# Optimization experiments

Measured on AMD Instinct MI355X. Metric: run time of the kernel, lower is better.

Reference implementation:

```python
import jax, jax.numpy as jnp
import numpy as np

N_NODES = 50000


def gcn_layer(x, src, dst, W, b):
    # GCNConv: out = D^{-1/2} (A + I) D^{-1/2} (x W) + b
    n = x.shape[0]
    h = x @ W  # [N, C_out]
    # degree including self-loop (count of incoming edges at dst + 1)
    deg = jnp.zeros((n,), dtype=x.dtype).at[dst].add(1.0) + 1.0
    dinv_sqrt = jax.lax.rsqrt(deg)
    norm = dinv_sqrt[src] * dinv_sqrt[dst]  # [E]
    agg = jax.ops.segment_sum(h[src] * norm[:, None], dst, num_segments=n)
    # self-loop contribution: norm_ii = 1/deg_i
    agg = agg + h * (dinv_sqrt * dinv_sqrt)[:, None]
    return agg + b


def setup_inputs() -> dict:
    key = jax.random.key(0)
    k1, k2, k3, k4, k5, k6 = jax.random.split(key, 6)
    in_c, hid_c, out_c = 128, 128, 64
    x = jax.random.normal(k1, (N_NODES, in_c), dtype=jnp.float32)
    edge_index = jax.random.randint(k2, (2, 600000), 0, N_NODES, dtype=jnp.int64)
    W1 = jax.random.normal(k3, (in_c, hid_c), dtype=jnp.float32) * (1.0 / np.sqrt(in_c))
    b1 = jnp.zeros((hid_c,), dtype=jnp.float32)
    W2 = jax.random.normal(k4, (hid_c, out_c), dtype=jnp.float32) * (1.0 / np.sqrt(hid_c))
    b2 = jnp.zeros((out_c,), dtype=jnp.float32)
    return {"x": x, "edge_index": edge_index, "W1": W1, "b1": b1, "W2": W2, "b2": b2}


def reference(x, edge_index, W1, b1, W2, b2):
    src, dst = edge_index[0], edge_index[1]
    h = gcn_layer(x, src, dst, W1, b1)
    h = jax.nn.relu(h)
    out = gcn_layer(h, src, dst, W2, b2)
    return out
```

## Files before the change

### kernel.cpp

```cpp
#include <hip/hip_runtime.h>

#define IN_C 128
#define HID_C 128
#define OUT_C 64
#define CAP 40
#define LSTR 40

typedef unsigned int uint;
typedef unsigned short ushort;
typedef __attribute__((ext_vector_type(8))) short short8;
typedef __attribute__((ext_vector_type(4))) float f32x4;

__device__ __forceinline__ float bf2f(ushort u) {
    return __uint_as_float(((uint)u) << 16);
}
__device__ __forceinline__ float bfl(uint u) {
    return __uint_as_float(u << 16);
}
__device__ __forceinline__ float bfh(uint u) {
    return __uint_as_float(u & 0xffff0000u);
}
__device__ __forceinline__ ushort f2bf(float f) {
    uint u = __float_as_uint(f);
    return (ushort)((u + 0x7fffu + ((u >> 16) & 1u)) >> 16);
}


__global__ void prep0_kernel(int* __restrict__ cursor, int n,
                             const float* __restrict__ W1, ushort* __restrict__ w1h,
                             ushort* __restrict__ w1l, const float* __restrict__ W2,
                             ushort* __restrict__ w2h, ushort* __restrict__ w2l) {
    int idx = blockIdx.x * blockDim.x + threadIdx.x;
    if (idx < n) {
        cursor[idx] = 0;
    } else if (idx < n + 128 * 128) {
        int i1 = idx - n;
        int k = i1 >> 7, c = i1 & 127;
        float w = W1[i1];
        ushort h = f2bf(w);
        ushort l = f2bf(w - bf2f(h));
        w1h[c * 128 + k] = h;
        w1l[c * 128 + k] = l;
    } else if (idx < n + 128 * 128 + 128 * 64) {
        int i2 = idx - n - 128 * 128;
        int k = i2 >> 6, c = i2 & 63;
        float w = W2[i2];
        ushort h = f2bf(w);
        ushort l = f2bf(w - bf2f(h));
        w2h[c * 128 + k] = h;
        w2l[c * 128 + k] = l;
    }
}


__global__ __launch_bounds__(256) void gemm1_edge_kernel(
    const float* __restrict__ A, const ushort* __restrict__ BTh,
    const ushort* __restrict__ BTl, ushort* __restrict__ C, int M, int gblocks,
    const int* __restrict__ src, const int* __restrict__ dst,
    int* __restrict__ cursor, int* __restrict__ csr_src, int E) {
    constexpr int BN = 128;
    constexpr int NT = BN / 16;
    __shared__ ushort sAh[64 * LSTR], sAl[64 * LSTR];
    __shared__ ushort sBh[BN * LSTR], sBl[BN * LSTR];

    const int tid = threadIdx.x;

    if (blockIdx.x >= gblocks) {
        int e = (blockIdx.x - gblocks) * 256 + tid;
        if (e < E) {
            unsigned s = (unsigned)src[e];
            unsigned d = (unsigned)dst[e];
            if (s < (unsigned)M && d < (unsigned)M) {
                int p = atomicAdd(&cursor[d], 1);
                if (p < CAP) csr_src[d * CAP + p] = (int)s;
            }
        }
        return;
    }

    const int w = tid >> 6;
    const int lane = tid & 63;
    const int m = lane & 15;
    const int quad = lane >> 4;
    const int r0 = blockIdx.x * 64;

    f32x4 acc[NT];
#pragma unroll
    for (int t = 0; t < NT; ++t) acc[t] = (f32x4){0.f, 0.f, 0.f, 0.f};

    for (int k0 = 0; k0 < 128; k0 += 32) {
#pragma unroll
        for (int it = 0; it < 2; ++it) {
            int idx = tid + it * 256;
            int row = idx >> 3;
            int c4 = idx & 7;
            int grow = r0 + row;
            float4 v = make_float4(0.f, 0.f, 0.f, 0.f);
            if (grow < M) v = *(const float4*)&A[(size_t)grow * 128 + k0 + c4 * 4];
            ushort h0 = f2bf(v.x), h1 = f2bf(v.y), h2 = f2bf(v.z), h3 = f2bf(v.w);
            ushort l0 = f2bf(v.x - bf2f(h0)), l1 = f2bf(v.y - bf2f(h1));
            ushort l2 = f2bf(v.z - bf2f(h2)), l3 = f2bf(v.w - bf2f(h3));
            *(ushort4*)&sAh[row * LSTR + c4 * 4] = make_ushort4(h0, h1, h2, h3);
            *(ushort4*)&sAl[row * LSTR + c4 * 4] = make_ushort4(l0, l1, l2, l3);
        }
        for (int idx = tid; idx < BN * 4; idx += 256) {
            int row = idx >> 2;
            int c = idx & 3;
            *(uint4*)&sBh[row * LSTR + c * 8] = *(const uint4*)&BTh[row * 128 + k0 + c * 8];
            *(uint4*)&sBl[row * LSTR + c * 8] = *(const uint4*)&BTl[row * 128 + k0 + c * 8];
        }
        __syncthreads();

        short8 ah = *(const short8*)&sAh[(w * 16 + m) * LSTR + quad * 8];
        short8 al = *(const short8*)&sAl[(w * 16 + m) * LSTR + quad * 8];
#pragma unroll
        for (int t = 0; t < NT; ++t) {
            short8 bh = *(const short8*)&sBh[(t * 16 + m) * LSTR + quad * 8];
            short8 bl = *(const short8*)&sBl[(t * 16 + m) * LSTR + quad * 8];
            acc[t] = __builtin_amdgcn_mfma_f32_16x16x32_bf16(ah, bh, acc[t], 0, 0, 0);
            acc[t] = __builtin_amdgcn_mfma_f32_16x16x32_bf16(al, bh, acc[t], 0, 0, 0);
            acc[t] = __builtin_amdgcn_mfma_f32_16x16x32_bf16(ah, bl, acc[t], 0, 0, 0);
        }
        __syncthreads();
    }

#pragma unroll
    for (int t = 0; t < NT; ++t) {
#pragma unroll
        for (int r = 0; r < 4; ++r) {
            int row = r0 + w * 16 + quad * 4 + r;
            if (row < M) C[(size_t)row * BN + t * 16 + m] = f2bf(acc[t][r]);
        }
    }
}


#define ACC8(v, nn)                                     \
    {                                                   \
        a0 += (nn) * bfl((v).x); a1 += (nn) * bfh((v).x); \
        a2 += (nn) * bfl((v).y); a3 += (nn) * bfh((v).y); \
        a4 += (nn) * bfl((v).z); a5 += (nn) * bfh((v).z); \
        a6 += (nn) * bfl((v).w); a7 += (nn) * bfh((v).w); \
    }


__global__ __launch_bounds__(256) void agg_gemm2_kernel(
    const uint4* __restrict__ hx, const int* __restrict__ csr_src,
    const int* __restrict__ degs, const float* __restrict__ bias,
    const ushort* __restrict__ BTh, const ushort* __restrict__ BTl,
    ushort* __restrict__ C, int n) {
    __shared__ ushort sAf[4][32][LSTR];

    const int tid = threadIdx.x;
    const int w = tid >> 6;
    const int lane = tid & 63;
    const int q4 = lane >> 4;
    const int c16 = lane & 15;
    const int r0 = blockIdx.x * 32;

    int nd = 0, t0 = 0, t1 = 0, t2 = 0;
    {
        int node = r0 + w * 8 + q4;
        bool valid = node < n;
        nd = valid ? degs[node] : 0;
        size_t base = (size_t)node * CAP;
        t0 = valid ? csr_src[base + c16] : 0;
        t1 = valid ? csr_src[base + 16 + c16] : 0;
        t2 = (valid && c16 < 8) ? csr_src[base + 32 + c16] : 0;
    }

    for (int g = 0; g < 2; ++g) {
        const int lrow = w * 8 + g * 4 + q4;
        const int node = r0 + lrow;
        const bool valid = node < n;
        const int cnt = min(nd, CAP);
        const float degf = (float)(cnt + 1);
        const float dinv = rsqrtf(degf);
        int es0 = (c16 < cnt) ? t0 : 0;
        int es1 = (16 + c16 < cnt) ? t1 : 0;
        int es2 = (32 + c16 < cnt) ? t2 : 0;
        int d0 = degs[es0];
        int d1 = degs[es1];
        int d2 = degs[es2];
        uint4 sv = make_uint4(0u, 0u, 0u, 0u);
        if (valid) sv = hx[(size_t)node * 16 + c16];
        int nd_n = 0, t0n = 0, t1n = 0, t2n = 0;
        if (g + 1 < 2) {
            int node_n = r0 + w * 8 + (g + 1) * 4 + q4;
            bool vn = node_n < n;
            nd_n = vn ? degs[node_n] : 0;
            size_t base_n = (size_t)node_n * CAP;
            t0n = vn ? csr_src[base_n + c16] : 0;
            t1n = vn ? csr_src[base_n + 16 + c16] : 0;
            t2n = (vn && c16 < 8) ? csr_src[base_n + 32 + c16] : 0;
        }
        float en0 = (c16 < cnt) ? rsqrtf((float)(d0 + 1)) * dinv : 0.f;
        float en1 = (16 + c16 < cnt) ? rsqrtf((float)(d1 + 1)) * dinv : 0.f;
        float en2 = (32 + c16 < cnt) ? rsqrtf((float)(d2 + 1)) * dinv : 0.f;
        int cm = cnt;
        cm = max(cm, __shfl_xor(cm, 16));
        cm = max(cm, __shfl_xor(cm, 32));

        float a0 = 0.f, a1 = 0.f, a2 = 0.f, a3 = 0.f;
        float a4 = 0.f, a5 = 0.f, a6 = 0.f, a7 = 0.f;

        auto EDGE = [&](int kk, int& s, float& wt) {
            if (kk < 16) {
                s = __shfl(es0, (q4 << 4) + kk);
                wt = __shfl(en0, (q4 << 4) + kk);
            } else if (kk < 32) {
                s = __shfl(es1, (q4 << 4) + kk - 16);
                wt = __shfl(en1, (q4 << 4) + kk - 16);
            } else {
                s = __shfl(es2, (q4 << 4) + kk - 32);
                wt = __shfl(en2, (q4 << 4) + kk - 32);
            }
        };

        int k = 0;
        for (; k + 2 <= cm; k += 2) {
            int sA; float nA; EDGE(k, sA, nA);
            int sB; float nB; EDGE(k + 1, sB, nB);
            uint4 vA = hx[(size_t)sA * 16 + c16];
            uint4 vB = hx[(size_t)sB * 16 + c16];
            ACC8(vA, nA);
            ACC8(vB, nB);
        }
        if (k < cm) {
            int sA; float nA; EDGE(k, sA, nA);
            uint4 vA = hx[(size_t)sA * 16 + c16];
            ACC8(vA, nA);
        }

        float sn = 1.0f / degf;
        const float4* b4 = (const float4*)bias;
        float4 bA = b4[2 * c16], bB = b4[2 * c16 + 1];
        float o0 = fmaxf(a0 + bfl(sv.x) * sn + bA.x, 0.f);
        float o1 = fmaxf(a1 + bfh(sv.x) * sn + bA.y, 0.f);
        float o2 = fmaxf(a2 + bfl(sv.y) * sn + bA.z, 0.f);
        float o3 = fmaxf(a3 + bfh(sv.y) * sn + bA.w, 0.f);
        float o4 = fmaxf(a4 + bfl(sv.z) * sn + bB.x, 0.f);
        float o5 = fmaxf(a5 + bfh(sv.z) * sn + bB.y, 0.f);
        float o6 = fmaxf(a6 + bfl(sv.w) * sn + bB.z, 0.f);
        float o7 = fmaxf(a7 + bfh(sv.w) * sn + bB.w, 0.f);
        uint4 u;
        u.x = (uint)f2bf(o0) | ((uint)f2bf(o1) << 16);
        u.y = (uint)f2bf(o2) | ((uint)f2bf(o3) << 16);
        u.z = (uint)f2bf(o4) | ((uint)f2bf(o5) << 16);
        u.w = (uint)f2bf(o6) | ((uint)f2bf(o7) << 16);
        *(uint4*)&sAf[c16 >> 2][lrow][(c16 & 3) * 8] = u;

        nd = nd_n; t0 = t0n; t1 = t1n; t2 = t2n;
    }

    const int wm = w >> 1;
    const int wn = w & 1;

    short8 rbh[4][2], rbl[4][2];
#pragma unroll
    for (int k0x = 0; k0x < 4; ++k0x) {
#pragma unroll
        for (int t = 0; t < 2; ++t) {
            int row = (wn * 2 + t) * 16 + c16;
            rbh[k0x][t] = *(const short8*)&BTh[(size_t)row * 128 + k0x * 32 + q4 * 8];
            rbl[k0x][t] = *(const short8*)&BTl[(size_t)row * 128 + k0x * 32 + q4 * 8];
        }
    }

    __syncthreads();

    f32x4 acc[2];
#pragma unroll
    for (int t = 0; t < 2; ++t) acc[t] = (f32x4){0.f, 0.f, 0.f, 0.f};

#pragma unroll
    for (int k0x = 0; k0x < 4; ++k0x) {
        short8 ah = *(const short8*)&sAf[k0x][wm * 16 + c16][q4 * 8];
#pragma unroll
        for (int t = 0; t < 2; ++t) {
            acc[t] = __builtin_amdgcn_mfma_f32_16x16x32_bf16(ah, rbh[k0x][t], acc[t], 0, 0, 0);
            acc[t] = __builtin_amdgcn_mfma_f32_16x16x32_bf16(ah, rbl[k0x][t], acc[t], 0, 0, 0);
        }
    }

#pragma unroll
    for (int t = 0; t < 2; ++t) {
#pragma unroll
        for (int r = 0; r < 4; ++r) {
            int row = r0 + wm * 16 + q4 * 4 + r;
            if (row < n) C[(size_t)row * 64 + (wn * 2 + t) * 16 + c16] = f2bf(acc[t][r]);
        }
    }
}


__global__ __launch_bounds__(256) void agg64_kernel(
    const uint4* __restrict__ hx, const int* __restrict__ csr_src,
    const int* __restrict__ degs, const float* __restrict__ bias,
    float* __restrict__ out, int n) {
    const int w = threadIdx.x >> 6;
    const int lane = threadIdx.x & 63;
    const int g = lane >> 3;
    const int q = lane & 7;
    const int node = blockIdx.x * 32 + w * 8 + g;
    const bool valid = node < n;

    int nd = valid ? degs[node] : 0;
    const int cnt = min(nd, CAP);
    const float dinv = rsqrtf((float)(cnt + 1));
    const size_t base = (size_t)node * CAP;

    int t0 = (valid && q < cnt) ? csr_src[base + q] : 0;
    int t1 = (valid && 8 + q < cnt) ? csr_src[base + 8 + q] : 0;
    int t2 = (valid && 16 + q < cnt) ? csr_src[base + 16 + q] : 0;
    int t3 = (valid && 24 + q < cnt) ? csr_src[base + 24 + q] : 0;
    int t4 = (valid && 32 + q < cnt) ? csr_src[base + 32 + q] : 0;
    int d0 = degs[t0], d1 = degs[t1], d2 = degs[t2], d3 = degs[t3], d4 = degs[t4];
    uint4 sv = make_uint4(0u, 0u, 0u, 0u);
    if (valid) sv = hx[(size_t)node * 8 + q];

    float e0 = (q < cnt) ? rsqrtf((float)(d0 + 1)) * dinv : 0.f;
    float e1 = (8 + q < cnt) ? rsqrtf((float)(d1 + 1)) * dinv : 0.f;
    float e2 = (16 + q < cnt) ? rsqrtf((float)(d2 + 1)) * dinv : 0.f;
    float e3 = (24 + q < cnt) ? rsqrtf((float)(d3 + 1)) * dinv : 0.f;
    float e4 = (32 + q < cnt) ? rsqrtf((float)(d4 + 1)) * dinv : 0.f;

    int cm = cnt;
    cm = max(cm, __shfl_xor(cm, 8));
    cm = max(cm, __shfl_xor(cm, 16));
    cm = max(cm, __shfl_xor(cm, 32));

    float a0 = 0.f, a1 = 0.f, a2 = 0.f, a3 = 0.f;
    float a4 = 0.f, a5 = 0.f, a6 = 0.f, a7 = 0.f;

    auto EDGE = [&](int kk, int& s, float& wt) {
        int sl = (g << 3) + (kk & 7);
        if (kk < 8)       { s = __shfl(t0, sl); wt = __shfl(e0, sl); }
        else if (kk < 16) { s = __shfl(t1, sl); wt = __shfl(e1, sl); }
        else if (kk < 24) { s = __shfl(t2, sl); wt = __shfl(e2, sl); }
        else if (kk < 32) { s = __shfl(t3, sl); wt = __shfl(e3, sl); }
        else              { s = __shfl(t4, sl); wt = __shfl(e4, sl); }
    };

    int k = 0;
    for (; k + 2 <= cm; k += 2) {
        int sA; float nA; EDGE(k, sA, nA);
        int sB; float nB; EDGE(k + 1, sB, nB);
        uint4 vA = hx[(size_t)sA * 8 + q];
        uint4 vB = hx[(size_t)sB * 8 + q];
        ACC8(vA, nA);
        ACC8(vB, nB);
    }
    if (k < cm) {
        int sA; float nA; EDGE(k, sA, nA);
        uint4 vA = hx[(size_t)sA * 8 + q];
        ACC8(vA, nA);
    }

    if (valid) {
        float sn = dinv * dinv;
        const float4* b4 = (const float4*)bias;
        float4 bA = b4[2 * q], bB = b4[2 * q + 1];
        float4 oA, oB;
        oA.x = a0 + bfl(sv.x) * sn + bA.x;
        oA.y = a1 + bfh(sv.x) * sn + bA.y;
        oA.z = a2 + bfl(sv.y) * sn + bA.z;
        oA.w = a3 + bfh(sv.y) * sn + bA.w;
        oB.x = a4 + bfl(sv.z) * sn + bB.x;
        oB.y = a5 + bfh(sv.z) * sn + bB.y;
        oB.z = a6 + bfl(sv.w) * sn + bB.z;
        oB.w = a7 + bfh(sv.w) * sn + bB.w;
        float4* o4 = (float4*)out;
        o4[(size_t)node * 16 + 2 * q] = oA;
        o4[(size_t)node * 16 + 2 * q + 1] = oB;
    }
}


extern "C" void kernel_launch(void* const* d_in, const int* in_sizes, int n_in,
                              void* d_out, int out_size, void* d_ws, size_t ws_size,
                              hipStream_t stream) {
    (void)n_in; (void)out_size; (void)ws_size;
    const float* x  = (const float*)d_in[0];
    const int*   ei = (const int*)d_in[1];
    const float* W1 = (const float*)d_in[2];
    const float* b1 = (const float*)d_in[3];
    const float* W2 = (const float*)d_in[4];
    const float* b2 = (const float*)d_in[5];
    float* out = (float*)d_out;

    const int n = in_sizes[0] / IN_C;
    const int E = in_sizes[1] / 2;
    const int* src = ei;
    const int* dst = ei + E;

    char* ws = (char*)d_ws;
    size_t off = 0;
    auto alloc = [&](size_t bytes) -> void* {
        void* p = ws + off;
        off += (bytes + 1023) & ~(size_t)1023;
        return p;
    };

    ushort* w1h     = (ushort*)alloc(128 * 128 * 2);
    ushort* w1l     = (ushort*)alloc(128 * 128 * 2);
    ushort* w2h     = (ushort*)alloc(64 * 128 * 2);
    ushort* w2l     = (ushort*)alloc(64 * 128 * 2);
    int*    cursor  = (int*)   alloc((size_t)n * 4);
    int*    csr_src = (int*)   alloc((size_t)n * CAP * 4);
    ushort* h1      = (ushort*)alloc((size_t)n * HID_C * 2);
    ushort* h2      = (ushort*)alloc((size_t)n * HID_C * 2);

    const int gblocks = (n + 63) / 64;
    const int EB = (E + 255) / 256;
    const int fblocks = (n + 31) / 32;

    prep0_kernel<<<(n + 128 * 128 + 128 * 64 + 255) / 256, 256, 0, stream>>>(
        cursor, n, W1, w1h, w1l, W2, w2h, w2l);
    gemm1_edge_kernel<<<gblocks + EB, 256, 0, stream>>>(x, w1h, w1l, h1, n, gblocks,
                                                        src, dst, cursor, csr_src, E);
    agg_gemm2_kernel<<<fblocks, 256, 0, stream>>>((const uint4*)h1, csr_src, cursor,
                                                  b1, w2h, w2l, h2, n);
    agg64_kernel<<<fblocks, 256, 0, stream>>>((const uint4*)h2, csr_src, cursor,
                                              b2, out, n);
}
```

Baseline: 170.6 us.

## Unroll gather loops by four, move barrier before weight loads, memset cursor

The neighbour-gather loops in both aggregation kernels now handle four edges per iteration, so more independent row loads are in flight. In agg_gemm2 the __syncthreads moves ahead of the B-fragment loads and gains a sched_barrier, which keeps the scheduler from interleaving those loads with the gather phase. Cursor zeroing leaves the prep kernel and becomes a hipMemsetAsync, shrinking the prep grid. The extra unrolling raises register pressure, and the memset adds a separate operation to the stream.

```diff
diff --git a/kernel.cpp b/kernel.cpp
--- a/kernel.cpp
+++ b/kernel.cpp
@@ -26,23 +26,19 @@
 }
 
 
-__global__ void prep0_kernel(int* __restrict__ cursor, int n,
-                             const float* __restrict__ W1, ushort* __restrict__ w1h,
+__global__ void prep0_kernel(const float* __restrict__ W1, ushort* __restrict__ w1h,
                              ushort* __restrict__ w1l, const float* __restrict__ W2,
                              ushort* __restrict__ w2h, ushort* __restrict__ w2l) {
     int idx = blockIdx.x * blockDim.x + threadIdx.x;
-    if (idx < n) {
-        cursor[idx] = 0;
-    } else if (idx < n + 128 * 128) {
-        int i1 = idx - n;
-        int k = i1 >> 7, c = i1 & 127;
-        float w = W1[i1];
+    if (idx < 128 * 128) {
+        int k = idx >> 7, c = idx & 127;
+        float w = W1[idx];
         ushort h = f2bf(w);
         ushort l = f2bf(w - bf2f(h));
         w1h[c * 128 + k] = h;
         w1l[c * 128 + k] = l;
-    } else if (idx < n + 128 * 128 + 128 * 64) {
-        int i2 = idx - n - 128 * 128;
+    } else if (idx < 128 * 128 + 128 * 64) {
+        int i2 = idx - 128 * 128;
         int k = i2 >> 6, c = i2 & 63;
         float w = W2[i2];
         ushort h = f2bf(w);
@@ -218,6 +214,20 @@
         };
 
         int k = 0;
+        for (; k + 4 <= cm; k += 4) {
+            int sA; float nA; EDGE(k, sA, nA);
+            int sB; float nB; EDGE(k + 1, sB, nB);
+            int sC; float nC; EDGE(k + 2, sC, nC);
+            int sD; float nD; EDGE(k + 3, sD, nD);
+            uint4 vA = hx[(size_t)sA * 16 + c16];
+            uint4 vB = hx[(size_t)sB * 16 + c16];
+            uint4 vC = hx[(size_t)sC * 16 + c16];
+            uint4 vD = hx[(size_t)sD * 16 + c16];
+            ACC8(vA, nA);
+            ACC8(vB, nB);
+            ACC8(vC, nC);
+            ACC8(vD, nD);
+        }
         for (; k + 2 <= cm; k += 2) {
             int sA; float nA; EDGE(k, sA, nA);
             int sB; float nB; EDGE(k + 1, sB, nB);
@@ -253,6 +263,9 @@
         nd = nd_n; t0 = t0n; t1 = t1n; t2 = t2n;
     }
 
+    __syncthreads();
+    __builtin_amdgcn_sched_barrier(0);
+
     const int wm = w >> 1;
     const int wn = w & 1;
 
@@ -266,8 +279,6 @@
             rbl[k0x][t] = *(const short8*)&BTl[(size_t)row * 128 + k0x * 32 + q4 * 8];
         }
     }
-
-    __syncthreads();
 
     f32x4 acc[2];
 #pragma unroll
@@ -343,6 +354,20 @@
     };
 
     int k = 0;
+    for (; k + 4 <= cm; k += 4) {
+        int sA; float nA; EDGE(k, sA, nA);
+        int sB; float nB; EDGE(k + 1, sB, nB);
+        int sC; float nC; EDGE(k + 2, sC, nC);
+        int sD; float nD; EDGE(k + 3, sD, nD);
+        uint4 vA = hx[(size_t)sA * 8 + q];
+        uint4 vB = hx[(size_t)sB * 8 + q];
+        uint4 vC = hx[(size_t)sC * 8 + q];
+        uint4 vD = hx[(size_t)sD * 8 + q];
+        ACC8(vA, nA);
+        ACC8(vB, nB);
+        ACC8(vC, nC);
+        ACC8(vD, nD);
+    }
     for (; k + 2 <= cm; k += 2) {
         int sA; float nA; EDGE(k, sA, nA);
         int sB; float nB; EDGE(k + 1, sB, nB);
@@ -415,8 +440,9 @@
     const int EB = (E + 255) / 256;
     const int fblocks = (n + 31) / 32;
 
-    prep0_kernel<<<(n + 128 * 128 + 128 * 64 + 255) / 256, 256, 0, stream>>>(
-        cursor, n, W1, w1h, w1l, W2, w2h, w2l);
+    hipMemsetAsync(cursor, 0, (size_t)n * 4, stream);
+    prep0_kernel<<<(128 * 128 + 128 * 64 + 255) / 256, 256, 0, stream>>>(
+        W1, w1h, w1l, W2, w2h, w2l);
     gemm1_edge_kernel<<<gblocks + EB, 256, 0, stream>>>(x, w1h, w1l, h1, n, gblocks,
                                                         src, dst, cursor, csr_src, E);
     agg_gemm2_kernel<<<fblocks, 256, 0, stream>>>((const uint4*)h1, csr_src, cursor,
```

Result: no change. 168.7 us (-1.1%).
